# Kernel tuning notes

Measured on AMD Instinct MI355X. Metric: run time of the kernel, lower is better.

The kernel has to match this reference:

```python
import jax, jax.numpy as jnp
import numpy as np


def _maxpool(x, win):
    return jax.lax.reduce_window(x, -jnp.inf, jax.lax.max, (1, 1) + win, (1, 1, 1, 1, 1), 'SAME')


def dilation26(x):
    return _maxpool(x, (3, 3, 3))


def dilation6(x):
    p1 = _maxpool(x, (3, 1, 1))
    p2 = _maxpool(x, (1, 3, 1))
    p3 = _maxpool(x, (1, 1, 3))
    return jnp.maximum(jnp.maximum(p1, p2), p3)


def erosion6(x):
    return -dilation6(-x)


def skeletonize3d(X, iters):
    # opening3d(X, conn_e=6, conn_d=26) = dilation26(erosion6(X)); persistent=True
    skel = jax.nn.relu(X - dilation26(erosion6(X)))
    for _ in range(iters):
        Xe = erosion6(X)
        delta = jax.nn.relu(Xe - dilation26(erosion6(Xe)))
        skel = X * dilation26(skel) + skel          # persistent reinforcement
        skel = skel + delta - skel * delta
        X = Xe
    # skel[skel>1] = skel/skel.detach() -> numerically 1.0
    return jnp.where(skel > 1.0, jnp.asarray(1.0, skel.dtype), skel)


def persistent_skeletonization3d(X, niter):
    return skeletonize3d(skeletonize3d(X, niter), niter // 2)


def _bmean_vs(v, s, eps):
    ax = (1, 2, 3, 4)
    return jnp.mean((jnp.sum(v * s, axis=ax) + eps) / (jnp.sum(s, axis=ax) + eps))


def ms_loss(Vlogit, Vcl, Vedt, k=5, eps=1e-12, bin_tresh=0.7):
    Vp = jax.nn.sigmoid(Vlogit)
    Vb = (jax.lax.stop_gradient(Vp) > bin_tresh).astype(Vp.dtype)
    Vb = jnp.pad(Vb, ((0, 0), (0, 0), (3, 3), (3, 3), (3, 3)), constant_values=1.0)
    S = persistent_skeletonization3d(Vb, k)[:, :, 3:-3, 3:-3, 3:-3]
    Sp = jax.lax.stop_gradient(S) * Vp
    tprec = _bmean_vs(Vp, Vcl, eps)
    tsens = _bmean_vs(Vcl, Sp, eps)
    return 1.0 - (2.0 * tprec * tsens + eps) / (tprec + tsens + eps)


def setup_inputs() -> dict:
    key = jax.random.key(0)
    k1, k2, k3 = jax.random.split(key, 3)
    B, C, D, H, W = 2, 1, 128, 128, 128
    Vlogit = jax.random.normal(k1, (B, C, D, H, W), dtype=jnp.float32)
    Vcl = jax.random.uniform(k2, (B, C, D, H, W), dtype=jnp.float32)
    Vedt = jax.random.uniform(k3, (B, C, D, H, W), dtype=jnp.float32)
    return {"Vlogit": Vlogit, "Vcl": Vcl, "Vedt": Vedt}


def reference(Vlogit, Vcl, Vedt):
    return ms_loss(Vlogit, Vcl, Vedt, k=5, eps=1e-12, bin_tresh=0.7)
```

## Files before the change

### kernel.cpp

```cpp
#include <hip/hip_runtime.h>
#include <stdint.h>

typedef unsigned long long u64;

#define PADW 134
#define WPR 3
#define ROWS_PER_B (PADW * PADW)
#define WPB (ROWS_PER_B * WPR)
#define NBATCH 2
#define NROWS (NBATCH * ROWS_PER_B)
#define NWORDS (NBATCH * WPB)
#define NV 128
#define NV3 (NV * NV * NV)
#define PAD 3
#define RBLK 512


__device__ __forceinline__ bool inR(int v) { return (unsigned)v < (unsigned)PADW; }

__device__ __forceinline__ void loadRow(const u64* __restrict__ B, int z, int y, u64 r[3]) {
  const u64* p = B + (z * PADW + y) * WPR;
  r[0] = p[0]; r[1] = p[1]; r[2] = p[2];
}

__device__ __forceinline__ void load3w(const u64* __restrict__ B, int z, int y, int j,
                                       u64 w[3]) {
  const u64* p = B + (z * PADW + y) * WPR;
  w[0] = j > 0 ? p[j - 1] : 0ULL;
  w[1] = p[j];
  w[2] = j < 2 ? p[j + 1] : 0ULL;
}

__device__ __forceinline__ u64 hdilw(const u64 w[3]) {
  return w[1] | (w[1] << 1) | (w[0] >> 63) | (w[1] >> 1) | (w[2] << 63);
}

__device__ __forceinline__ u64 herow(const u64 w[3], int j) {
  u64 lin = (j == 0) ? 1ULL : (w[0] >> 63);
  u64 rin = (j == 2) ? (1ULL << 5) : (w[2] << 63);
  return w[1] & ((w[1] << 1) | lin) & ((w[1] >> 1) | rin);
}

__device__ __forceinline__ void eroX(const u64 c[3], u64 e[3]) {
  e[0] = c[0] & ((c[0] << 1) | 1ULL)         & ((c[0] >> 1) | (c[1] << 63));
  e[1] = c[1] & ((c[1] << 1) | (c[0] >> 63)) & ((c[1] >> 1) | (c[2] << 63));
  e[2] = c[2] & ((c[2] << 1) | (c[1] >> 63)) & ((c[2] >> 1) | (1ULL << 5));
}

__device__ __forceinline__ u64 selj(u64 r0, u64 r1, u64 r2, int j) {
  return (j == 0) ? r0 : ((j == 1) ? r1 : r2);
}

__device__ __forceinline__ u64 hdilj(u64 r0, u64 r1, u64 r2, int j) {
  u64 a  = selj(r0, r1, r2, j);
  u64 am = (j == 0) ? 0ULL : ((j == 1) ? r0 : r1);
  u64 ap = (j == 2) ? 0ULL : ((j == 0) ? r1 : r2);
  return a | (a << 1) | (am >> 63) | (a >> 1) | (ap << 63);
}

__device__ __forceinline__ void decompW(int idx, int& b, int& z, int& y, int& j) {
  b = idx / WPB;
  int r = idx - b * WPB;
  z = r / (PADW * WPR);
  int r2 = r - z * (PADW * WPR);
  y = r2 / WPR;
  j = r2 - y * WPR;
}

__device__ __forceinline__ void eroRowFull(const u64* __restrict__ Bb, int z, int y,
                                           u64 e[3]) {
  u64 c[3], n[3];
  loadRow(Bb, z, y, c);
  eroX(c, e);
  if (inR(y - 1)) { loadRow(Bb, z, y - 1, n); e[0] &= n[0]; e[1] &= n[1]; e[2] &= n[2]; }
  if (inR(y + 1)) { loadRow(Bb, z, y + 1, n); e[0] &= n[0]; e[1] &= n[1]; e[2] &= n[2]; }
  if (inR(z - 1)) { loadRow(Bb, z - 1, y, n); e[0] &= n[0]; e[1] &= n[1]; e[2] &= n[2]; }
  if (inR(z + 1)) { loadRow(Bb, z + 1, y, n); e[0] &= n[0]; e[1] &= n[1]; e[2] &= n[2]; }
}

__global__ void binpack_k(const float* __restrict__ logit, u64* __restrict__ X) {
  int wid = (blockIdx.x * blockDim.x + threadIdx.x) >> 6;
  int lane = threadIdx.x & 63;
  if (wid >= NROWS) return;
  int b = wid / ROWS_PER_B;
  int r = wid - b * ROWS_PER_B;
  int z = r / PADW;
  int y = r - z * PADW;
  bool padrow = (z < PAD || z >= PAD + NV || y < PAD || y >= PAD + NV);
  const float TH = 0.84729786f;
  u64* rowp = X + (size_t)b * WPB + (z * PADW + y) * WPR;
#pragma unroll
  for (int j = 0; j < WPR; ++j) {
    int x = j * 64 + lane;
    bool pred = false;
    if (x < PADW) {
      if (padrow || x < PAD || x >= PAD + NV) {
        pred = true;
      } else {
        float l = logit[(((size_t)b * NV + (z - PAD)) * NV + (y - PAD)) * NV + (x - PAD)];
        pred = l > TH;
      }
    }
    u64 w = __ballot(pred);
    if (lane == 0) rowp[j] = w;
  }
}

__global__ __launch_bounds__(256) void initf_k(const u64* __restrict__ X,
                                               u64* __restrict__ E1out,
                                               u64* __restrict__ E2out,
                                               u64* __restrict__ skout) {
  int idx = blockIdx.x * blockDim.x + threadIdx.x;
  if (idx >= NWORDS) return;
  int b, z, y, j;
  decompW(idx, b, z, y, j);
  const u64* Xb = X + (size_t)b * WPB;
  u64 dil = 0;
  u64 c30 = 0, c31 = 0, c32 = 0;
  u64 ecross = ~0ULL;
#pragma unroll
  for (int dz = -1; dz <= 1; ++dz) {
#pragma unroll
    for (int dy = -1; dy <= 1; ++dy) {
      int zz = z + dz, yy = y + dy;
      if (!inR(zz) || !inR(yy)) continue;
      u64 er[3];
      eroRowFull(Xb, zz, yy, er);
      dil |= hdilj(er[0], er[1], er[2], j);
      if (dz == 0 && dy == 0) { c30 = er[0]; c31 = er[1]; c32 = er[2]; }
      else if (dz * dz + dy * dy == 1) ecross &= selj(er[0], er[1], er[2], j);
    }
  }
  u64 wm = (j == 0) ? 0ULL : ((j == 1) ? c30 : c31);
  u64 wc = selj(c30, c31, c32, j);
  u64 wp = (j == 2) ? 0ULL : ((j == 0) ? c31 : c32);
  u64 lin = (j == 0) ? 1ULL : (wm >> 63);
  u64 rin = (j == 2) ? (1ULL << 5) : (wp << 63);
  u64 e2 = wc & ((wc << 1) | lin) & ((wc >> 1) | rin);
  e2 &= ecross;

  E1out[idx] = wc;
  E2out[idx] = e2;
  skout[idx] = Xb[(z * PADW + y) * WPR + j] & ~dil;
}

__global__ __launch_bounds__(256) void upd_k(const u64* __restrict__ X,
                                             const u64* __restrict__ E1,
                                             const u64* __restrict__ E2,
                                             const u64* __restrict__ sk,
                                             u64* __restrict__ sk2,
                                             u64* __restrict__ E3) {
  int idx = blockIdx.x * blockDim.x + threadIdx.x;
  if (idx >= NWORDS) return;
  int b, z, y, j;
  decompW(idx, b, z, y, j);
  size_t boff = (size_t)b * WPB;
  const u64* Eb = E2 + boff;
  const u64* Sb = sk + boff;
  u64 acc = 0, dsk = 0;
  u64 cc3[3], skcw = 0;
  u64 ecross = ~0ULL;
#pragma unroll
  for (int dz = -1; dz <= 1; ++dz) {
#pragma unroll
    for (int dy = -1; dy <= 1; ++dy) {
      int zz = z + dz, yy = y + dy;
      if (!inR(zz) || !inR(yy)) continue;
      u64 t3[3], s3[3];
      load3w(Eb, zz, yy, j, t3);
      load3w(Sb, zz, yy, j, s3);
      acc |= hdilw(t3);
      dsk |= hdilw(s3);
      if (dz == 0 && dy == 0) {
        cc3[0] = t3[0]; cc3[1] = t3[1]; cc3[2] = t3[2];
        skcw = s3[1];
      } else if (dz * dz + dy * dy == 1) {
        ecross &= t3[1];
      }
    }
  }
  u64 e = herow(cc3, j) & ecross;
  u64 delta = E1[idx] & ~acc;
  u64 s1 = (X[idx] & dsk) | skcw;
  sk2[idx] = delta | s1;
  E3[idx] = e;
}

__global__ __launch_bounds__(256) void reduce1_k(const float* __restrict__ logit,
                                                 const float* __restrict__ vcl,
                                                 const u64* __restrict__ S,
                                                 float* __restrict__ partials) {
  int tid = blockIdx.x * 256 + threadIdx.x;
  float p[8];
#pragma unroll
  for (int k = 0; k < 8; ++k) p[k] = 0.f;
  for (int s = tid; s < NV3 / 4; s += RBLK * 256) {
    int i = s << 2;
    int z = i >> 14, y = (i >> 7) & 127, x = i & 127;
#pragma unroll
    for (int b = 0; b < NBATCH; ++b) {
      float4 lv = ((const float4*)(logit + (size_t)b * NV3))[s];
      float4 cv = ((const float4*)(vcl + (size_t)b * NV3))[s];
      const u64* rowp = S + (size_t)b * WPB + ((size_t)(z + PAD) * PADW + (y + PAD)) * WPR;
      float lf[4] = {lv.x, lv.y, lv.z, lv.w};
      float cf[4] = {cv.x, cv.y, cv.z, cv.w};
#pragma unroll
      for (int k = 0; k < 4; ++k) {
        float vp = 1.0f / (1.0f + expf(-lf[k]));
        int xp = x + k + PAD;
        u64 w = rowp[xp >> 6];
        float sv = (float)((w >> (xp & 63)) & 1ULL);
        float c = cf[k];
        p[b * 4 + 0] += vp * c;
        p[b * 4 + 1] += c;
        p[b * 4 + 2] += c * vp * sv;
        p[b * 4 + 3] += vp * sv;
      }
    }
  }
#pragma unroll
  for (int k = 0; k < 8; ++k)
    for (int off = 32; off > 0; off >>= 1) p[k] += __shfl_down(p[k], off);
  __shared__ float ls[4][8];
  int wid = threadIdx.x >> 6, lane = threadIdx.x & 63;
  if (lane == 0) {
#pragma unroll
    for (int k = 0; k < 8; ++k) ls[wid][k] = p[k];
  }
  __syncthreads();
  if (threadIdx.x == 0) {
#pragma unroll
    for (int k = 0; k < 8; ++k)
      partials[k * RBLK + blockIdx.x] = ls[0][k] + ls[1][k] + ls[2][k] + ls[3][k];
  }
}

__global__ void finalize2_k(const float* __restrict__ partials, float* __restrict__ out) {
  int t = threadIdx.x;
  double s[8];
#pragma unroll
  for (int k = 0; k < 8; ++k) s[k] = (double)partials[k * RBLK + t];
#pragma unroll
  for (int k = 0; k < 8; ++k)
    for (int off = 32; off > 0; off >>= 1) s[k] += __shfl_down(s[k], off);
  __shared__ double ls[8][8];
  int wid = t >> 6, lane = t & 63;
  if (lane == 0) {
#pragma unroll
    for (int k = 0; k < 8; ++k) ls[k][wid] = s[k];
  }
  __syncthreads();
  if (t == 0) {
    double a[8];
#pragma unroll
    for (int k = 0; k < 8; ++k) {
      a[k] = 0.0;
      for (int w = 0; w < 8; ++w) a[k] += ls[k][w];
    }
    const double eps = 1e-12;
    double tp = 0.5 * ((a[0] + eps) / (a[1] + eps) + (a[4] + eps) / (a[5] + eps));
    double ts = 0.5 * ((a[2] + eps) / (a[3] + eps) + (a[6] + eps) / (a[7] + eps));
    out[0] = (float)(1.0 - (2.0 * tp * ts + eps) / (tp + ts + eps));
  }
}

extern "C" void kernel_launch(void* const* d_in, const int* in_sizes, int n_in,
                              void* d_out, int out_size, void* d_ws, size_t ws_size,
                              hipStream_t stream) {
  const float* logit = (const float*)d_in[0];
  const float* vcl = (const float*)d_in[1];
  float* out = (float*)d_out;

  const size_t bufW = (size_t)NWORDS;
  u64* base = (u64*)d_ws;
  u64* B[6];
  for (int i = 0; i < 6; ++i) B[i] = base + (size_t)i * bufW;
  float* partials = (float*)(base + 6 * bufW);

  const int mThreads = 256;
  const int mBlocks = (NWORDS + mThreads - 1) / mThreads;
  const int bBlocks = (NROWS + 3) / 4;

  binpack_k<<<bBlocks, 256, 0, stream>>>(logit, B[0]);

  u64 *X = B[0], *E1 = B[1], *E2 = B[2], *E3 = B[3], *sk = B[4], *sk2 = B[5];
  initf_k<<<mBlocks, mThreads, 0, stream>>>(X, E1, E2, sk);
  for (int it = 0; it < 5; ++it) {
    upd_k<<<mBlocks, mThreads, 0, stream>>>(X, E1, E2, sk, sk2, E3);
    u64* t = X; X = E1; E1 = E2; E2 = E3; E3 = t;
    t = sk; sk = sk2; sk2 = t;
  }
  u64* S1 = sk;

  u64 *X2 = S1, *E1b = X, *E2b = E1, *E3b = E2, *skb = E3, *sk2b = sk2;
  initf_k<<<mBlocks, mThreads, 0, stream>>>(X2, E1b, E2b, skb);
  for (int it = 0; it < 2; ++it) {
    upd_k<<<mBlocks, mThreads, 0, stream>>>(X2, E1b, E2b, skb, sk2b, E3b);
    u64* t = X2; X2 = E1b; E1b = E2b; E2b = E3b; E3b = t;
    t = skb; skb = sk2b; sk2b = t;
  }
  u64* Sfinal = skb;

  reduce1_k<<<RBLK, 256, 0, stream>>>(logit, vcl, Sfinal, partials);
  finalize2_k<<<1, 512, 0, stream>>>(partials, out);
}
```

Baseline: 179.3 us.

## Fuse erosion chains per row and evolve skeleton in LDS-tiled kernel

Replaces the per-word init/update kernels with two new kernels. The first, run per row, computes three successive 6-connected erosions at once by keeping neighbour rows in registers. The second evolves the skeleton over all iterations inside one tiled block, with halo-extended tiles held in shared memory. This cuts the kernel launch count and the global round-trips of the skeleton between iterations. In exchange it recomputes halos and makes each row thread do heavy register work (a 5x5x3 array of erosion rows), which may lower occupancy.

```diff
diff --git a/kernel.cpp b/kernel.cpp
--- a/kernel.cpp
+++ b/kernel.cpp
@@ -14,6 +14,7 @@
 #define NV3 (NV * NV * NV)
 #define PAD 3
 #define RBLK 512
+#define TS 16
 
 
 __device__ __forceinline__ bool inR(int v) { return (unsigned)v < (unsigned)PADW; }
@@ -23,22 +24,16 @@
   r[0] = p[0]; r[1] = p[1]; r[2] = p[2];
 }
 
-__device__ __forceinline__ void load3w(const u64* __restrict__ B, int z, int y, int j,
-                                       u64 w[3]) {
-  const u64* p = B + (z * PADW + y) * WPR;
-  w[0] = j > 0 ? p[j - 1] : 0ULL;
-  w[1] = p[j];
-  w[2] = j < 2 ? p[j + 1] : 0ULL;
-}
-
-__device__ __forceinline__ u64 hdilw(const u64 w[3]) {
-  return w[1] | (w[1] << 1) | (w[0] >> 63) | (w[1] >> 1) | (w[2] << 63);
-}
-
-__device__ __forceinline__ u64 herow(const u64 w[3], int j) {
-  u64 lin = (j == 0) ? 1ULL : (w[0] >> 63);
-  u64 rin = (j == 2) ? (1ULL << 5) : (w[2] << 63);
-  return w[1] & ((w[1] << 1) | lin) & ((w[1] >> 1) | rin);
+__device__ __forceinline__ bool rowRead(const u64* __restrict__ B, int gz, int gy, u64 r[3]) {
+  if (!inR(gz) || !inR(gy)) { r[0] = r[1] = r[2] = 0ULL; return false; }
+  loadRow(B, gz, gy, r);
+  return true;
+}
+
+__device__ __forceinline__ void orHdil(const u64 r[3], u64 d[3]) {
+  d[0] |= r[0] | (r[0] << 1) | ((r[0] >> 1) | (r[1] << 63));
+  d[1] |= r[1] | ((r[1] << 1) | (r[0] >> 63)) | ((r[1] >> 1) | (r[2] << 63));
+  d[2] |= r[2] | ((r[2] << 1) | (r[1] >> 63)) | (r[2] >> 1);
 }
 
 __device__ __forceinline__ void eroX(const u64 c[3], u64 e[3]) {
@@ -47,35 +42,23 @@
   e[2] = c[2] & ((c[2] << 1) | (c[1] >> 63)) & ((c[2] >> 1) | (1ULL << 5));
 }
 
-__device__ __forceinline__ u64 selj(u64 r0, u64 r1, u64 r2, int j) {
-  return (j == 0) ? r0 : ((j == 1) ? r1 : r2);
-}
-
-__device__ __forceinline__ u64 hdilj(u64 r0, u64 r1, u64 r2, int j) {
-  u64 a  = selj(r0, r1, r2, j);
-  u64 am = (j == 0) ? 0ULL : ((j == 1) ? r0 : r1);
-  u64 ap = (j == 2) ? 0ULL : ((j == 0) ? r1 : r2);
-  return a | (a << 1) | (am >> 63) | (a >> 1) | (ap << 63);
-}
-
-__device__ __forceinline__ void decompW(int idx, int& b, int& z, int& y, int& j) {
-  b = idx / WPB;
-  int r = idx - b * WPB;
-  z = r / (PADW * WPR);
-  int r2 = r - z * (PADW * WPR);
-  y = r2 / WPR;
-  j = r2 - y * WPR;
-}
-
-__device__ __forceinline__ void eroRowFull(const u64* __restrict__ Bb, int z, int y,
-                                           u64 e[3]) {
+__device__ __forceinline__ void eroAt(const u64* __restrict__ Bb, int gz, int gy, u64 e[3]) {
+  if (!inR(gz) || !inR(gy)) { e[0] = e[1] = e[2] = ~0ULL; return; }
   u64 c[3], n[3];
-  loadRow(Bb, z, y, c);
+  loadRow(Bb, gz, gy, c);
   eroX(c, e);
-  if (inR(y - 1)) { loadRow(Bb, z, y - 1, n); e[0] &= n[0]; e[1] &= n[1]; e[2] &= n[2]; }
-  if (inR(y + 1)) { loadRow(Bb, z, y + 1, n); e[0] &= n[0]; e[1] &= n[1]; e[2] &= n[2]; }
-  if (inR(z - 1)) { loadRow(Bb, z - 1, y, n); e[0] &= n[0]; e[1] &= n[1]; e[2] &= n[2]; }
-  if (inR(z + 1)) { loadRow(Bb, z + 1, y, n); e[0] &= n[0]; e[1] &= n[1]; e[2] &= n[2]; }
+  if (inR(gy - 1)) { loadRow(Bb, gz, gy - 1, n); e[0] &= n[0]; e[1] &= n[1]; e[2] &= n[2]; }
+  if (inR(gy + 1)) { loadRow(Bb, gz, gy + 1, n); e[0] &= n[0]; e[1] &= n[1]; e[2] &= n[2]; }
+  if (inR(gz - 1)) { loadRow(Bb, gz - 1, gy, n); e[0] &= n[0]; e[1] &= n[1]; e[2] &= n[2]; }
+  if (inR(gz + 1)) { loadRow(Bb, gz + 1, gy, n); e[0] &= n[0]; e[1] &= n[1]; e[2] &= n[2]; }
+}
+
+__device__ __forceinline__ void eroReg(const u64 c[3], const u64 ym[3], const u64 yp[3],
+                                       const u64 zm[3], const u64 zp[3], u64 e[3]) {
+  eroX(c, e);
+  e[0] &= ym[0] & yp[0] & zm[0] & zp[0];
+  e[1] &= ym[1] & yp[1] & zm[1] & zp[1];
+  e[2] &= ym[2] & yp[2] & zm[2] & zp[2];
 }
 
 __global__ void binpack_k(const float* __restrict__ logit, u64* __restrict__ X) {
@@ -106,84 +89,126 @@
   }
 }
 
-__global__ __launch_bounds__(256) void initf_k(const u64* __restrict__ X,
-                                               u64* __restrict__ E1out,
-                                               u64* __restrict__ E2out,
-                                               u64* __restrict__ skout) {
-  int idx = blockIdx.x * blockDim.x + threadIdx.x;
-  if (idx >= NWORDS) return;
-  int b, z, y, j;
-  decompW(idx, b, z, y, j);
-  const u64* Xb = X + (size_t)b * WPB;
-  u64 dil = 0;
-  u64 c30 = 0, c31 = 0, c32 = 0;
-  u64 ecross = ~0ULL;
+__global__ __launch_bounds__(256) void chain3_k(const u64* __restrict__ in,
+                                                u64* __restrict__ o1,
+                                                u64* __restrict__ o2,
+                                                u64* __restrict__ o3) {
+  int rid = blockIdx.x * 256 + threadIdx.x;
+  if (rid >= NROWS) return;
+  int b = rid / ROWS_PER_B;
+  int rr = rid - b * ROWS_PER_B;
+  int z = rr / PADW;
+  int y = rr - (rr / PADW) * PADW;
+  const u64* Bb = in + (size_t)b * WPB;
+
+  u64 e1[5][5][3];
+#pragma unroll
+  for (int dz = -2; dz <= 2; ++dz) {
+#pragma unroll
+    for (int dy = -2; dy <= 2; ++dy) {
+      int ad = (dz < 0 ? -dz : dz) + (dy < 0 ? -dy : dy);
+      if (ad > 2) continue;
+      eroAt(Bb, z + dz, y + dy, e1[dz + 2][dy + 2]);
+    }
+  }
+  u64 e2[3][3][3];
 #pragma unroll
   for (int dz = -1; dz <= 1; ++dz) {
 #pragma unroll
     for (int dy = -1; dy <= 1; ++dy) {
-      int zz = z + dz, yy = y + dy;
-      if (!inR(zz) || !inR(yy)) continue;
-      u64 er[3];
-      eroRowFull(Xb, zz, yy, er);
-      dil |= hdilj(er[0], er[1], er[2], j);
-      if (dz == 0 && dy == 0) { c30 = er[0]; c31 = er[1]; c32 = er[2]; }
-      else if (dz * dz + dy * dy == 1) ecross &= selj(er[0], er[1], er[2], j);
-    }
-  }
-  u64 wm = (j == 0) ? 0ULL : ((j == 1) ? c30 : c31);
-  u64 wc = selj(c30, c31, c32, j);
-  u64 wp = (j == 2) ? 0ULL : ((j == 0) ? c31 : c32);
-  u64 lin = (j == 0) ? 1ULL : (wm >> 63);
-  u64 rin = (j == 2) ? (1ULL << 5) : (wp << 63);
-  u64 e2 = wc & ((wc << 1) | lin) & ((wc >> 1) | rin);
-  e2 &= ecross;
-
-  E1out[idx] = wc;
-  E2out[idx] = e2;
-  skout[idx] = Xb[(z * PADW + y) * WPR + j] & ~dil;
-}
-
-__global__ __launch_bounds__(256) void upd_k(const u64* __restrict__ X,
-                                             const u64* __restrict__ E1,
-                                             const u64* __restrict__ E2,
-                                             const u64* __restrict__ sk,
-                                             u64* __restrict__ sk2,
-                                             u64* __restrict__ E3) {
-  int idx = blockIdx.x * blockDim.x + threadIdx.x;
-  if (idx >= NWORDS) return;
-  int b, z, y, j;
-  decompW(idx, b, z, y, j);
+      int ad = (dz < 0 ? -dz : dz) + (dy < 0 ? -dy : dy);
+      if (ad > 1) continue;
+      if (!inR(z + dz) || !inR(y + dy)) {
+        e2[dz + 1][dy + 1][0] = e2[dz + 1][dy + 1][1] = e2[dz + 1][dy + 1][2] = ~0ULL;
+      } else {
+        eroReg(e1[dz + 2][dy + 2], e1[dz + 2][dy + 1], e1[dz + 2][dy + 3],
+               e1[dz + 1][dy + 2], e1[dz + 3][dy + 2], e2[dz + 1][dy + 1]);
+      }
+    }
+  }
+  u64 e3[3];
+  eroReg(e2[1][1], e2[1][0], e2[1][2], e2[0][1], e2[2][1], e3);
+
+  size_t off = (size_t)b * WPB + (z * PADW + y) * WPR;
+  o1[off + 0] = e1[2][2][0]; o1[off + 1] = e1[2][2][1]; o1[off + 2] = e1[2][2][2];
+  o2[off + 0] = e2[1][1][0]; o2[off + 1] = e2[1][1][1]; o2[off + 2] = e2[1][1][2];
+  o3[off + 0] = e3[0];       o3[off + 1] = e3[1];       o3[off + 2] = e3[2];
+}
+
+struct EPtrs { const u64* p[7]; };
+
+template<int ITERS>
+__global__ __launch_bounds__(512) void skevo_k(EPtrs eps, u64* __restrict__ Sg) {
+  constexpr int H = ITERS;
+  constexpr int SW = TS + 2 * H;
+  constexpr int R = SW * SW;
+  __shared__ u64 lds[2][R][3];
+  const int nt = (PADW + TS - 1) / TS;
+  int b = blockIdx.x / (nt * nt);
+  int t = blockIdx.x - b * (nt * nt);
+  int z0 = (t / nt) * TS - H;
+  int y0 = (t - (t / nt) * nt) * TS - H;
   size_t boff = (size_t)b * WPB;
-  const u64* Eb = E2 + boff;
-  const u64* Sb = sk + boff;
-  u64 acc = 0, dsk = 0;
-  u64 cc3[3], skcw = 0;
-  u64 ecross = ~0ULL;
-#pragma unroll
-  for (int dz = -1; dz <= 1; ++dz) {
-#pragma unroll
-    for (int dy = -1; dy <= 1; ++dy) {
-      int zz = z + dz, yy = y + dy;
-      if (!inR(zz) || !inR(yy)) continue;
-      u64 t3[3], s3[3];
-      load3w(Eb, zz, yy, j, t3);
-      load3w(Sb, zz, yy, j, s3);
-      acc |= hdilw(t3);
-      dsk |= hdilw(s3);
-      if (dz == 0 && dy == 0) {
-        cc3[0] = t3[0]; cc3[1] = t3[1]; cc3[2] = t3[2];
-        skcw = s3[1];
-      } else if (dz * dz + dy * dy == 1) {
-        ecross &= t3[1];
+
+  for (int ir = threadIdx.x; ir < R; ir += 512) {
+    int gz = z0 + ir / SW, gy = y0 + ir % SW;
+    u64 d[3] = {0, 0, 0}, rr[3], c[3];
+#pragma unroll
+    for (int dz = -1; dz <= 1; ++dz)
+#pragma unroll
+      for (int dy = -1; dy <= 1; ++dy)
+        if (rowRead(eps.p[1] + boff, gz + dz, gy + dy, rr)) orHdil(rr, d);
+    rowRead(eps.p[0] + boff, gz, gy, c);
+    lds[0][ir][0] = c[0] & ~d[0];
+    lds[0][ir][1] = c[1] & ~d[1];
+    lds[0][ir][2] = c[2] & ~d[2];
+  }
+  __syncthreads();
+
+  int cur = 0;
+#pragma unroll
+  for (int it = 1; it <= ITERS; ++it) {
+    for (int ir = threadIdx.x; ir < R; ir += 512) {
+      int iz = ir / SW, iy = ir - (ir / SW) * SW;
+      int gz = z0 + iz, gy = y0 + iy;
+      u64 dE[3] = {0, 0, 0}, dS[3] = {0, 0, 0}, rr[3];
+#pragma unroll
+      for (int dz = -1; dz <= 1; ++dz) {
+#pragma unroll
+        for (int dy = -1; dy <= 1; ++dy) {
+          if (rowRead(eps.p[it + 1] + boff, gz + dz, gy + dy, rr)) orHdil(rr, dE);
+          int jz = iz + dz, jy = iy + dy;
+          if (jz >= 0 && jz < SW && jy >= 0 && jy < SW) {
+            u64 sr[3];
+            sr[0] = lds[cur][jz * SW + jy][0];
+            sr[1] = lds[cur][jz * SW + jy][1];
+            sr[2] = lds[cur][jz * SW + jy][2];
+            orHdil(sr, dS);
+          }
+        }
       }
-    }
-  }
-  u64 e = herow(cc3, j) & ecross;
-  u64 delta = E1[idx] & ~acc;
-  u64 s1 = (X[idx] & dsk) | skcw;
-  sk2[idx] = delta | s1;
-  E3[idx] = e;
+      u64 ec[3], xc[3];
+      rowRead(eps.p[it] + boff, gz, gy, ec);
+      rowRead(eps.p[it - 1] + boff, gz, gy, xc);
+      u64 s0 = lds[cur][ir][0], s1 = lds[cur][ir][1], s2 = lds[cur][ir][2];
+      lds[cur ^ 1][ir][0] = (ec[0] & ~dE[0]) | s0 | (xc[0] & dS[0]);
+      lds[cur ^ 1][ir][1] = (ec[1] & ~dE[1]) | s1 | (xc[1] & dS[1]);
+      lds[cur ^ 1][ir][2] = (ec[2] & ~dE[2]) | s2 | (xc[2] & dS[2]);
+    }
+    __syncthreads();
+    cur ^= 1;
+  }
+
+  for (int ir = threadIdx.x; ir < R; ir += 512) {
+    int iz = ir / SW, iy = ir - (ir / SW) * SW;
+    if (iz < H || iz >= H + TS || iy < H || iy >= H + TS) continue;
+    int gz = z0 + iz, gy = y0 + iy;
+    if (!inR(gz) || !inR(gy)) continue;
+    u64* o = Sg + boff + (gz * PADW + gy) * WPR;
+    o[0] = lds[cur][ir][0];
+    o[1] = lds[cur][ir][1];
+    o[2] = lds[cur][ir][2];
+  }
 }
 
 __global__ __launch_bounds__(256) void reduce1_k(const float* __restrict__ logit,
@@ -271,36 +296,30 @@
   const float* vcl = (const float*)d_in[1];
   float* out = (float*)d_out;
 
-  const size_t bufW = (size_t)NWORDS;
   u64* base = (u64*)d_ws;
-  u64* B[6];
-  for (int i = 0; i < 6; ++i) B[i] = base + (size_t)i * bufW;
-  float* partials = (float*)(base + 6 * bufW);
-
-  const int mThreads = 256;
-  const int mBlocks = (NWORDS + mThreads - 1) / mThreads;
+  u64* B[8];
+  for (int i = 0; i < 8; ++i) B[i] = base + (size_t)i * NWORDS;
+  float* partials = (float*)(base + (size_t)8 * NWORDS);
+
+  const int cBlocks = (NROWS + 255) / 256;
+  const int nt = (PADW + TS - 1) / TS;
+  const int sBlocks = NBATCH * nt * nt;
   const int bBlocks = (NROWS + 3) / 4;
 
   binpack_k<<<bBlocks, 256, 0, stream>>>(logit, B[0]);
 
-  u64 *X = B[0], *E1 = B[1], *E2 = B[2], *E3 = B[3], *sk = B[4], *sk2 = B[5];
-  initf_k<<<mBlocks, mThreads, 0, stream>>>(X, E1, E2, sk);
-  for (int it = 0; it < 5; ++it) {
-    upd_k<<<mBlocks, mThreads, 0, stream>>>(X, E1, E2, sk, sk2, E3);
-    u64* t = X; X = E1; E1 = E2; E2 = E3; E3 = t;
-    t = sk; sk = sk2; sk2 = t;
-  }
-  u64* S1 = sk;
-
-  u64 *X2 = S1, *E1b = X, *E2b = E1, *E3b = E2, *skb = E3, *sk2b = sk2;
-  initf_k<<<mBlocks, mThreads, 0, stream>>>(X2, E1b, E2b, skb);
-  for (int it = 0; it < 2; ++it) {
-    upd_k<<<mBlocks, mThreads, 0, stream>>>(X2, E1b, E2b, skb, sk2b, E3b);
-    u64* t = X2; X2 = E1b; E1b = E2b; E2b = E3b; E3b = t;
-    t = skb; skb = sk2b; sk2b = t;
-  }
-  u64* Sfinal = skb;
-
-  reduce1_k<<<RBLK, 256, 0, stream>>>(logit, vcl, Sfinal, partials);
+  chain3_k<<<cBlocks, 256, 0, stream>>>(B[0], B[1], B[2], B[3]);
+  chain3_k<<<cBlocks, 256, 0, stream>>>(B[3], B[4], B[5], B[6]);
+  EPtrs eA;
+  for (int i = 0; i < 7; ++i) eA.p[i] = B[i];
+  skevo_k<5><<<sBlocks, 512, 0, stream>>>(eA, B[7]);
+
+  chain3_k<<<cBlocks, 256, 0, stream>>>(B[7], B[1], B[2], B[3]);
+  EPtrs eB;
+  eB.p[0] = B[7]; eB.p[1] = B[1]; eB.p[2] = B[2]; eB.p[3] = B[3];
+  eB.p[4] = B[0]; eB.p[5] = B[0]; eB.p[6] = B[0];
+  skevo_k<2><<<sBlocks, 512, 0, stream>>>(eB, B[4]);
+
+  reduce1_k<<<RBLK, 256, 0, stream>>>(logit, vcl, B[4], partials);
   finalize2_k<<<1, 512, 0, stream>>>(partials, out);
 }
```

Result: slower. 191.2 us (+6.7%).
